# Performance work log

Measured on AMD Instinct MI355X. Metric: run time of the kernel, lower is better.

Reference implementation:

```python
import jax, jax.numpy as jnp
import numpy as np

KS = 3          # deform kernel size
N = KS * KS     # 9 sampling taps per pixel
PAD = 1         # zero padding applied before sampling (nn.ZeroPad2d)
BN_EPS = 1e-5


def conv2d(x, w, b=None, stride=1, padding=0):
    out = jax.lax.conv_general_dilated(
        x, w, (stride, stride), [(padding, padding)] * 2,
        dimension_numbers=('NCHW', 'OIHW', 'NCHW'))
    if b is not None:
        out = out + b[None, :, None, None]
    return out


def setup_inputs() -> dict:
    key = jax.random.key(0)
    ks = jax.random.split(key, 6)
    inC, outC = 128, 256
    B, H, W = 8, 64, 64

    def kaiming(k, shape):
        fan_in = shape[1] * shape[2] * shape[3]
        return jax.random.normal(k, shape, jnp.float32) / np.float32(np.sqrt(fan_in))

    return {
        'x': jax.random.normal(ks[0], (B, inC, H, W), jnp.float32),
        'w_offset': kaiming(ks[1], (2 * N, inC, 3, 3)) * 0.1,  # small offsets, realistic
        'b_offset': jnp.zeros((2 * N,), jnp.float32),
        'w_mask': kaiming(ks[2], (N, inC, 3, 3)),
        'b_mask': jnp.zeros((N,), jnp.float32),
        'w_conv': kaiming(ks[3], (outC, inC, KS, KS)),
        'bn_gamma': jnp.ones((outC,), jnp.float32),
        'bn_beta': jnp.zeros((outC,), jnp.float32),
        'bn_mean': jax.random.normal(ks[4], (outC,), jnp.float32) * 0.1,
        'bn_var': jnp.ones((outC,), jnp.float32) + jax.random.uniform(ks[5], (outC,), jnp.float32) * 0.1,
    }


def deform_conv(x, w_offset, b_offset, w_mask, b_mask, w_conv):
    B, C, H, W = x.shape
    dt = x.dtype

    offset = conv2d(x, w_offset, b_offset, 1, 1)               # (B, 2N, H, W)
    m = jax.nn.sigmoid(conv2d(x, w_mask, b_mask, 1, 1))        # (B, N, H, W)

    # kernel grid offsets p_n (first N channels = rows, last N = cols)
    rng = jnp.arange(-(KS - 1) // 2, (KS - 1) // 2 + 1, dtype=dt)
    pnx, pny = jnp.meshgrid(rng, rng, indexing='ij')
    p_n = jnp.concatenate([pnx.reshape(-1), pny.reshape(-1)])[None, :, None, None]

    # base positions p_0 (torch impl starts at 1, sampling on padded input)
    p0x = jnp.broadcast_to(jnp.arange(1, H + 1, dtype=dt)[:, None], (H, W))
    p0y = jnp.broadcast_to(jnp.arange(1, W + 1, dtype=dt)[None, :], (H, W))
    p_0 = jnp.concatenate([jnp.tile(p0x[None], (N, 1, 1)),
                           jnp.tile(p0y[None], (N, 1, 1))])[None]  # (1, 2N, H, W)

    p = (offset + p_n + p_0).transpose(0, 2, 3, 1)             # (B, H, W, 2N)

    xp = jnp.pad(x, ((0, 0), (0, 0), (PAD, PAD), (PAD, PAD)))
    Hp, Wp = H + 2 * PAD, W + 2 * PAD

    px, py = p[..., :N], p[..., N:]
    fx, fy = jnp.floor(px), jnp.floor(py)
    q_lt_x = jnp.clip(fx, 0, Hp - 1)
    q_lt_y = jnp.clip(fy, 0, Wp - 1)
    q_rb_x = jnp.clip(fx + 1, 0, Hp - 1)
    q_rb_y = jnp.clip(fy + 1, 0, Wp - 1)
    px = jnp.clip(px, 0, Hp - 1)
    py = jnp.clip(py, 0, Wp - 1)

    # bilinear weights (faithful to the reference torch formulas)
    g_lt = (1 + (q_lt_x - px)) * (1 + (q_lt_y - py))
    g_rb = (1 - (q_rb_x - px)) * (1 - (q_rb_y - py))
    g_lb = (1 + (q_lt_x - px)) * (1 - (q_rb_y - py))
    g_rt = (1 - (q_rb_x - px)) * (1 + (q_lt_y - py))

    xp_flat = xp.reshape(B, C, Hp * Wp)

    def gather(qx, qy):
        idx = (qx.astype(jnp.int32) * Wp + qy.astype(jnp.int32)).reshape(B, 1, -1)
        out = jnp.take_along_axis(xp_flat,
                                  jnp.broadcast_to(idx, (B, C, idx.shape[-1])), axis=2)
        return out.reshape(B, C, H, W, N)

    x_off = (g_lt[:, None] * gather(q_lt_x, q_lt_y)
             + g_rb[:, None] * gather(q_rb_x, q_rb_y)
             + g_lb[:, None] * gather(q_lt_x, q_rb_y)
             + g_rt[:, None] * gather(q_rb_x, q_lt_y))       # (B, C, H, W, N)

    x_off = x_off * m.transpose(0, 2, 3, 1)[:, None]          # modulation

    # (B,C,H,W,ks,ks) -> (B,C,H*ks,W*ks)  (equivalent to _reshape_x_offset)
    x_off = x_off.reshape(B, C, H, W, KS, KS).transpose(0, 1, 2, 4, 3, 5)
    x_off = x_off.reshape(B, C, H * KS, W * KS)

    return conv2d(x_off, w_conv, None, KS, 0)                 # (B, outC, H, W)


def reference(x, w_offset, b_offset, w_mask, b_mask, w_conv,
              bn_gamma, bn_beta, bn_mean, bn_var):
    y = deform_conv(x, w_offset, b_offset, w_mask, b_mask, w_conv)
    inv = jax.lax.rsqrt(bn_var + BN_EPS)
    scale = (bn_gamma * inv)[None, :, None, None]
    shift = (bn_beta - bn_mean * bn_gamma * inv)[None, :, None, None]
    return jax.nn.relu(y * scale + shift)
```

## Files before the change

### kernel.cpp

```cpp
#include <hip/hip_runtime.h>
#include <math.h>

#define BB 8
#define CC 128
#define HH 64
#define WW 64
#define NPTS 9
#define OUTC 256
#define HW (HH*WW)
#define KTOT (CC*NPTS)
#define BK 288
#define AP 290
#define WROWS 6

typedef __attribute__((ext_vector_type(8))) short bf16x8;
typedef __attribute__((ext_vector_type(4))) float f32x4;

__device__ unsigned short g_wT[OUTC * KTOT];
__device__ unsigned short g_woT[32 * KTOT];

__device__ __forceinline__ unsigned short f2bf(float f) {
    unsigned int u = __builtin_bit_cast(unsigned int, f);
    unsigned int r = (u + 0x7FFFu + ((u >> 16) & 1u)) >> 16;
    return (unsigned short)r;
}

__device__ __forceinline__ unsigned cvtpk(float lo, float hi) {
    unsigned r;
    asm("v_cvt_pk_bf16_f32 %0, %1, %2" : "=v"(r) : "v"(lo), "v"(hi));
    return r;
}
__device__ __forceinline__ float bflo(unsigned w) { return __builtin_bit_cast(float, w << 16); }
__device__ __forceinline__ float bfhi(unsigned w) { return __builtin_bit_cast(float, w & 0xFFFF0000u); }

__device__ __forceinline__ int orig_k(int k) {
    int cb = k / BK, r = k % BK;
    int pair = r / 18, r2 = r % 18;
    int n = r2 >> 1, half = r2 & 1;
    return (cb * 32 + pair * 2 + half) * NPTS + n;
}

__global__ __launch_bounds__(256) void prep_kernel(
    const float* __restrict__ wo, const float* __restrict__ wm,
    const float* __restrict__ wc)
{
    int idx = blockIdx.x * 256 + threadIdx.x;
    const int T1 = 32 * KTOT;
    if (idx < T1) {
        int nn = idx / KTOT, k = idx - nn * KTOT;
        int ok = orig_k(k);
        float v = (nn < 18) ? wo[nn * KTOT + ok]
                            : (nn < 27 ? wm[(nn - 18) * KTOT + ok] : 0.f);
        g_woT[idx] = f2bf(v);
    } else if (idx < T1 + OUTC * KTOT) {
        int j = idx - T1;
        int oc = j / KTOT, k = j - oc * KTOT;
        g_wT[j] = f2bf(wc[oc * KTOT + orig_k(k)]);
    }
}

struct PF { uint2 w[WROWS]; };

__device__ __forceinline__ void issue(PF& pf, const float* __restrict__ xb,
                                      int h, int cb, int tid) {
    if (cb < 0 || cb > 3) return;
    int q = tid >> 6, col = tid & 63;
    const float* base = xb + (size_t)(cb * 32 + 4 * q) * HW + col;
    #pragma unroll
    for (int r = 0; r < WROWS; ++r) {
        int gr = h - 2 + r;
        bool v = (gr >= 0) & (gr < HH);
        float a0 = v ? base[0 * HW + gr * WW] : 0.f;
        float a1 = v ? base[1 * HW + gr * WW] : 0.f;
        float a2 = v ? base[2 * HW + gr * WW] : 0.f;
        float a3 = v ? base[3 * HW + gr * WW] : 0.f;
        pf.w[r].x = cvtpk(a0, a1);
        pf.w[r].y = cvtpk(a2, a3);
    }
}

__device__ __forceinline__ void commit(uint2* win, const PF& pf, int tid) {
    uint2* wp = win + (tid >> 6) * 384 + (tid & 63);
    #pragma unroll
    for (int r = 0; r < WROWS; ++r) wp[r * 64] = pf.w[r];
}

__global__ __launch_bounds__(512) __attribute__((amdgpu_waves_per_eu(4, 4)))
void fused_kernel(
    const float* __restrict__ x,
    const float* __restrict__ b_offset, const float* __restrict__ b_mask,
    const float* __restrict__ bn_gamma, const float* __restrict__ bn_beta,
    const float* __restrict__ bn_mean,  const float* __restrict__ bn_var,
    float* __restrict__ out)
{
    __shared__ unsigned short Atile[64][AP];
    __shared__ uint2 win[8 * 384];
    __shared__ float4 gtab[NPTS][64];
    __shared__ uint2  otab[NPTS][64];
    float* ovf = (float*)&Atile[0][0];

    int bid = blockIdx.x;
    int blk = (bid & 7) * 64 + (bid >> 3);
    int b = blk >> 6, h = blk & 63;
    int tid  = threadIdx.x;
    int lane = tid & 63;
    int wv   = __builtin_amdgcn_readfirstlane(tid >> 6);
    int l15  = lane & 15;
    int kg   = lane >> 4;
    int spix = lane;

    const float* xb = x + (size_t)b * CC * HW;
    unsigned* AtU = (unsigned*)&Atile[0][0];

    int mi_a = wv & 3, nf_a = wv >> 2;
    f32x4 s1acc = {0.f, 0.f, 0.f, 0.f};

    PF pf; issue(pf, xb, h, 0, tid);
    for (int cb = 0; cb < 4; ++cb) {
        commit(win, pf, tid);
        {
            const uint2* base = win + wv * 384;
            #pragma unroll
            for (int tap = 0; tap < 9; ++tap) {
                int ky = tap / 3, kx = tap % 3;
                int col  = spix + kx - 1;
                int colc = min(max(col, 0), WW - 1);
                uint2 v = base[(ky + 1) * 64 + colc];
                bool cv = (col >= 0) & (col < WW);
                AtU[spix * 145 + (2 * wv) * 9 + tap]     = cv ? v.x : 0u;
                AtU[spix * 145 + (2 * wv + 1) * 9 + tap] = cv ? v.y : 0u;
            }
        }
        issue(pf, xb, h, (cb < 3) ? cb + 1 : 2, tid);
        __syncthreads();
        __builtin_amdgcn_s_setprio(1);
        for (int q = 0; q < 9; ++q) {
            int koff = q * 32 + kg * 8;
            bf16x8 af = *(const bf16x8*)&Atile[mi_a * 16 + l15][koff];
            int nn = nf_a * 16 + l15;
            bf16x8 bfr = *(const bf16x8*)&g_woT[nn * KTOT + cb * BK + koff];
            s1acc = __builtin_amdgcn_mfma_f32_16x16x32_bf16(af, bfr, s1acc, 0, 0, 0);
        }
        __builtin_amdgcn_s_setprio(0);
        __syncthreads();
    }

    #pragma unroll
    for (int j = 0; j < 4; ++j) {
        float val = s1acc[j];
        int nn   = nf_a * 16 + l15;
        int pixl = mi_a * 16 + kg * 4 + j;
        if (nn < 9) {
            ovf[nn * 64 + pixl] = val + b_offset[nn] + (float)(nn / 3 - 1) + (float)(h + 1);
        } else if (nn < 18) {
            int n = nn - 9;
            ovf[576 + n * 64 + pixl] = val + b_offset[nn] + (float)(n % 3 - 1) + (float)(pixl + 1);
        } else if (nn < 27) {
            int n = nn - 18;
            float sg = val + b_mask[n];
            ovf[1152 + n * 64 + pixl] = 1.f / (1.f + expf(-sg));
        }
    }
    __syncthreads();

    for (int n = wv; n < NPTS; n += 8) {
        int t = lane;
        float px = ovf[n * 64 + t];
        float py = ovf[576 + n * 64 + t];
        float m  = ovf[1152 + n * 64 + t];
        float fx = floorf(px), fy = floorf(py);
        float qltx = fminf(fmaxf(fx,       0.f), 65.f);
        float qlty = fminf(fmaxf(fy,       0.f), 65.f);
        float qrbx = fminf(fmaxf(fx + 1.f, 0.f), 65.f);
        float qrby = fminf(fmaxf(fy + 1.f, 0.f), 65.f);
        float pxc  = fminf(fmaxf(px, 0.f), 65.f);
        float pyc  = fminf(fmaxf(py, 0.f), 65.f);
        float glt = (1.f + (qltx - pxc)) * (1.f + (qlty - pyc)) * m;
        float grb = (1.f - (qrbx - pxc)) * (1.f - (qrby - pyc)) * m;
        float glb = (1.f + (qltx - pxc)) * (1.f - (qrby - pyc)) * m;
        float grt = (1.f - (qrbx - pxc)) * (1.f + (qlty - pyc)) * m;
        int i0 = (int)qltx - 1, j0 = (int)qlty - 1;
        int i1 = (int)qrbx - 1, j1 = (int)qrby - 1;
        bool v00 = (i0 >= 0) & (i0 < HH) & (j0 >= 0) & (j0 < WW);
        bool v11 = (i1 >= 0) & (i1 < HH) & (j1 >= 0) & (j1 < WW);
        bool v01 = (i0 >= 0) & (i0 < HH) & (j1 >= 0) & (j1 < WW);
        bool v10 = (i1 >= 0) & (i1 < HH) & (j0 >= 0) & (j0 < WW);
        float4 g;
        g.x = v00 ? glt : 0.f;
        g.y = v11 ? grb : 0.f;
        g.z = v01 ? glb : 0.f;
        g.w = v10 ? grt : 0.f;
        gtab[n][t] = g;
        bool okr0 = ((i0 >= h - 2) & (i0 <= h + 3)) | !(v00 | v01);
        bool okr1 = ((i1 >= h - 2) & (i1 <= h + 3)) | !(v11 | v10);
        bool ok = okr0 & okr1;
        int r0w = min(max(i0 - (h - 2), 0), WROWS - 1);
        int r1w = min(max(i1 - (h - 2), 0), WROWS - 1);
        int r0g = min(max(i0, 0), HH - 1);
        int r1g = min(max(i1, 0), HH - 1);
        int j0c = min(max(j0, 0), WW - 1);
        int j1c = min(max(j1, 0), WW - 1);
        int o  = ok ? (r0w * WW + j0c) : (r0g * WW + j0c);
        int dr = ok ? (r1w - r0w) : (r1g - r0g);
        int dj = j1c - j0c;
        unsigned o00 = (unsigned)o;
        unsigned o11 = (unsigned)(o + dr * WW + dj);
        unsigned o01 = (unsigned)(o + dj);
        unsigned o10 = (unsigned)(o + dr * WW);
        uint2 ot;
        ot.x = (o00 | (ok ? 0u : 0x8000u)) | (o11 << 16);
        ot.y = o01 | (o10 << 16);
        otab[n][t] = ot;
    }
    __syncthreads();

    f32x4 acc[4][2];
    #pragma unroll
    for (int mi = 0; mi < 4; ++mi)
        #pragma unroll
        for (int ni = 0; ni < 2; ++ni)
            acc[mi][ni] = (f32x4){0.f, 0.f, 0.f, 0.f};

    int oc0 = wv * 32;

    for (int j = 0; j < 4; ++j) {
        int cb = 3 - j;
        if (j > 0) {
            commit(win, pf, tid);
            issue(pf, xb, h, cb - 1, tid);
        }
        {
            const uint2* baseq = win + wv * 384;
            const float* xg = xb + (size_t)(cb * 32 + 4 * wv) * HW;
            #pragma unroll
            for (int n = 0; n < NPTS; ++n) {
                float4 g  = gtab[n][spix];
                uint2  ot = otab[n][spix];
                int o00 = ot.x & 0x7FFF;
                int o11 = ot.x >> 16;
                int o01 = ot.y & 0xFFFF;
                int o10 = ot.y >> 16;
                float v0, v1, v2, v3;
                if (!(ot.x & 0x8000u)) {
                    uint2 c00 = baseq[o00];
                    uint2 c11 = baseq[o11];
                    uint2 c01 = baseq[o01];
                    uint2 c10 = baseq[o10];
                    v0 =       g.x * bflo(c00.x);
                    v0 = fmaf(g.y, bflo(c11.x), v0);
                    v0 = fmaf(g.z, bflo(c01.x), v0);
                    v0 = fmaf(g.w, bflo(c10.x), v0);
                    v1 =       g.x * bfhi(c00.x);
                    v1 = fmaf(g.y, bfhi(c11.x), v1);
                    v1 = fmaf(g.z, bfhi(c01.x), v1);
                    v1 = fmaf(g.w, bfhi(c10.x), v1);
                    v2 =       g.x * bflo(c00.y);
                    v2 = fmaf(g.y, bflo(c11.y), v2);
                    v2 = fmaf(g.z, bflo(c01.y), v2);
                    v2 = fmaf(g.w, bflo(c10.y), v2);
                    v3 =       g.x * bfhi(c00.y);
                    v3 = fmaf(g.y, bfhi(c11.y), v3);
                    v3 = fmaf(g.z, bfhi(c01.y), v3);
                    v3 = fmaf(g.w, bfhi(c10.y), v3);
                } else {
                    const float* x0 = xg;
                    const float* x1 = xg + HW;
                    const float* x2 = xg + 2 * HW;
                    const float* x3 = xg + 3 * HW;
                    v0 = g.x*x0[o00]; v0 = fmaf(g.y, x0[o11], v0); v0 = fmaf(g.z, x0[o01], v0); v0 = fmaf(g.w, x0[o10], v0);
                    v1 = g.x*x1[o00]; v1 = fmaf(g.y, x1[o11], v1); v1 = fmaf(g.z, x1[o01], v1); v1 = fmaf(g.w, x1[o10], v1);
                    v2 = g.x*x2[o00]; v2 = fmaf(g.y, x2[o11], v2); v2 = fmaf(g.z, x2[o01], v2); v2 = fmaf(g.w, x2[o10], v2);
                    v3 = g.x*x3[o00]; v3 = fmaf(g.y, x3[o11], v3); v3 = fmaf(g.z, x3[o01], v3); v3 = fmaf(g.w, x3[o10], v3);
                }
                AtU[spix * 145 + (2 * wv) * 9 + n]     = cvtpk(v0, v1);
                AtU[spix * 145 + (2 * wv + 1) * 9 + n] = cvtpk(v2, v3);
            }
        }
        __syncthreads();
        __builtin_amdgcn_s_setprio(1);
        for (int q = 0; q < 9; ++q) {
            int koff = q * 32 + kg * 8;
            bf16x8 af[4];
            #pragma unroll
            for (int mi = 0; mi < 4; ++mi)
                af[mi] = *(const bf16x8*)&Atile[mi * 16 + l15][koff];
            #pragma unroll
            for (int ni = 0; ni < 2; ++ni) {
                int oc = oc0 + ni * 16 + l15;
                bf16x8 bfr = *(const bf16x8*)&g_wT[oc * KTOT + cb * BK + koff];
                #pragma unroll
                for (int mi = 0; mi < 4; ++mi)
                    acc[mi][ni] = __builtin_amdgcn_mfma_f32_16x16x32_bf16(af[mi], bfr, acc[mi][ni], 0, 0, 0);
            }
        }
        __builtin_amdgcn_s_setprio(0);
        __syncthreads();
    }

    #pragma unroll
    for (int ni = 0; ni < 2; ++ni) {
        int oc = oc0 + ni * 16 + l15;
        float inv   = 1.f / sqrtf(bn_var[oc] + 1e-5f);
        float scale = bn_gamma[oc] * inv;
        float shift = bn_beta[oc] - bn_mean[oc] * scale;
        float* op = out + ((size_t)b * OUTC + oc) * HW + h * WW + kg * 4;
        #pragma unroll
        for (int mi = 0; mi < 4; ++mi) {
            f32x4 o4;
            #pragma unroll
            for (int j = 0; j < 4; ++j) {
                float v = fmaf(acc[mi][ni][j], scale, shift);
                o4[j] = v > 0.f ? v : 0.f;
            }
            *(f32x4*)(op + mi * 16) = o4;
        }
    }
}

extern "C" void kernel_launch(void* const* d_in, const int* in_sizes, int n_in,
                              void* d_out, int out_size, void* d_ws, size_t ws_size,
                              hipStream_t stream) {
    (void)in_sizes; (void)n_in; (void)out_size; (void)d_ws; (void)ws_size;
    const float* x        = (const float*)d_in[0];
    const float* w_offset = (const float*)d_in[1];
    const float* b_offset = (const float*)d_in[2];
    const float* w_mask   = (const float*)d_in[3];
    const float* b_mask   = (const float*)d_in[4];
    const float* w_conv   = (const float*)d_in[5];
    const float* bn_gamma = (const float*)d_in[6];
    const float* bn_beta  = (const float*)d_in[7];
    const float* bn_mean  = (const float*)d_in[8];
    const float* bn_var   = (const float*)d_in[9];
    float* out = (float*)d_out;

    int prep_elems = 32 * KTOT + OUTC * KTOT;
    prep_kernel<<<(prep_elems + 255) / 256, 256, 0, stream>>>(w_offset, w_mask, w_conv);
    fused_kernel<<<BB * HH, 512, 0, stream>>>(x, b_offset, b_mask,
                                              bn_gamma, bn_beta, bn_mean, bn_var, out);
}
```

Before: 81.29 us.

## Split each output row across two blocks of 32 pixels for more parallelism

Each block now handles half of an output row (32 pixels) instead of the full 64, doubling the grid to 1024 blocks. Each wave now builds two channels for 32 pixels instead of four channels for 64 pixels, and only four waves run the offset/mask MFMA stage. Shared memory per block shrinks, and the waves-per-EU hint is relaxed to allow more occupancy. The cost is that the input window load and the weight B-fragment reads are duplicated across the two halves, and each wave now does half as many MFMAs per B-fragment load.

```diff
diff --git a/kernel.cpp b/kernel.cpp
--- a/kernel.cpp
+++ b/kernel.cpp
@@ -85,7 +85,7 @@
     for (int r = 0; r < WROWS; ++r) wp[r * 64] = pf.w[r];
 }
 
-__global__ __launch_bounds__(512) __attribute__((amdgpu_waves_per_eu(4, 4)))
+__global__ __launch_bounds__(512) __attribute__((amdgpu_waves_per_eu(4, 8)))
 void fused_kernel(
     const float* __restrict__ x,
     const float* __restrict__ b_offset, const float* __restrict__ b_mask,
@@ -93,130 +93,139 @@
     const float* __restrict__ bn_mean,  const float* __restrict__ bn_var,
     float* __restrict__ out)
 {
-    __shared__ unsigned short Atile[64][AP];
+    __shared__ unsigned short Atile[32][AP];
     __shared__ uint2 win[8 * 384];
-    __shared__ float4 gtab[NPTS][64];
-    __shared__ uint2  otab[NPTS][64];
+    __shared__ float4 gtab[NPTS][32];
+    __shared__ uint2  otab[NPTS][32];
     float* ovf = (float*)&Atile[0][0];
 
     int bid = blockIdx.x;
-    int blk = (bid & 7) * 64 + (bid >> 3);
-    int b = blk >> 6, h = blk & 63;
+    int b = bid & 7;
+    int rr = bid >> 3;
+    int h = rr >> 1, half = rr & 1;
     int tid  = threadIdx.x;
     int lane = tid & 63;
     int wv   = __builtin_amdgcn_readfirstlane(tid >> 6);
     int l15  = lane & 15;
     int kg   = lane >> 4;
-    int spix = lane;
+    int p    = lane & 31;
+    int ps   = lane >> 5;
+    int pairIdx = wv * 2 + ps;
 
     const float* xb = x + (size_t)b * CC * HW;
     unsigned* AtU = (unsigned*)&Atile[0][0];
-
-    int mi_a = wv & 3, nf_a = wv >> 2;
+    const unsigned* wu = (const unsigned*)(win + wv * 384);
+
+    int mi_a = wv & 1, nf_a = (wv >> 1) & 1;
     f32x4 s1acc = {0.f, 0.f, 0.f, 0.f};
 
     PF pf; issue(pf, xb, h, 0, tid);
     for (int cb = 0; cb < 4; ++cb) {
         commit(win, pf, tid);
         {
-            const uint2* base = win + wv * 384;
             #pragma unroll
             for (int tap = 0; tap < 9; ++tap) {
                 int ky = tap / 3, kx = tap % 3;
-                int col  = spix + kx - 1;
-                int colc = min(max(col, 0), WW - 1);
-                uint2 v = base[(ky + 1) * 64 + colc];
-                bool cv = (col >= 0) & (col < WW);
-                AtU[spix * 145 + (2 * wv) * 9 + tap]     = cv ? v.x : 0u;
-                AtU[spix * 145 + (2 * wv + 1) * 9 + tap] = cv ? v.y : 0u;
+                int gcol = half * 32 + p + kx - 1;
+                int colc = min(max(gcol, 0), WW - 1);
+                unsigned w = wu[((ky + 1) * 64 + colc) * 2 + ps];
+                w = (gcol >= 0 && gcol < WW) ? w : 0u;
+                AtU[p * 145 + pairIdx * 9 + tap] = w;
             }
         }
         issue(pf, xb, h, (cb < 3) ? cb + 1 : 2, tid);
         __syncthreads();
         __builtin_amdgcn_s_setprio(1);
-        for (int q = 0; q < 9; ++q) {
-            int koff = q * 32 + kg * 8;
-            bf16x8 af = *(const bf16x8*)&Atile[mi_a * 16 + l15][koff];
-            int nn = nf_a * 16 + l15;
-            bf16x8 bfr = *(const bf16x8*)&g_woT[nn * KTOT + cb * BK + koff];
-            s1acc = __builtin_amdgcn_mfma_f32_16x16x32_bf16(af, bfr, s1acc, 0, 0, 0);
+        if (wv < 4) {
+            for (int q = 0; q < 9; ++q) {
+                int koff = q * 32 + kg * 8;
+                bf16x8 af = *(const bf16x8*)&Atile[mi_a * 16 + l15][koff];
+                int nn = nf_a * 16 + l15;
+                bf16x8 bfr = *(const bf16x8*)&g_woT[nn * KTOT + cb * BK + koff];
+                s1acc = __builtin_amdgcn_mfma_f32_16x16x32_bf16(af, bfr, s1acc, 0, 0, 0);
+            }
         }
         __builtin_amdgcn_s_setprio(0);
         __syncthreads();
     }
 
+    if (wv < 4) {
+        #pragma unroll
+        for (int j = 0; j < 4; ++j) {
+            float val = s1acc[j];
+            int nn   = nf_a * 16 + l15;
+            int pixl = mi_a * 16 + kg * 4 + j;
+            if (nn < 9) {
+                ovf[nn * 32 + pixl] = val + b_offset[nn] + (float)(nn / 3 - 1) + (float)(h + 1);
+            } else if (nn < 18) {
+                int n = nn - 9;
+                ovf[288 + n * 32 + pixl] = val + b_offset[nn] + (float)(n % 3 - 1)
+                                         + (float)(half * 32 + pixl + 1);
+            } else if (nn < 27) {
+                int n = nn - 18;
+                float sg = val + b_mask[n];
+                ovf[576 + n * 32 + pixl] = 1.f / (1.f + expf(-sg));
+            }
+        }
+    }
+    __syncthreads();
+
+    for (int n = wv; n < NPTS; n += 8) {
+        if (lane < 32) {
+            int t = lane;
+            float px = ovf[n * 32 + t];
+            float py = ovf[288 + n * 32 + t];
+            float m  = ovf[576 + n * 32 + t];
+            float fx = floorf(px), fy = floorf(py);
+            float qltx = fminf(fmaxf(fx,       0.f), 65.f);
+            float qlty = fminf(fmaxf(fy,       0.f), 65.f);
+            float qrbx = fminf(fmaxf(fx + 1.f, 0.f), 65.f);
+            float qrby = fminf(fmaxf(fy + 1.f, 0.f), 65.f);
+            float pxc  = fminf(fmaxf(px, 0.f), 65.f);
+            float pyc  = fminf(fmaxf(py, 0.f), 65.f);
+            float glt = (1.f + (qltx - pxc)) * (1.f + (qlty - pyc)) * m;
+            float grb = (1.f - (qrbx - pxc)) * (1.f - (qrby - pyc)) * m;
+            float glb = (1.f + (qltx - pxc)) * (1.f - (qrby - pyc)) * m;
+            float grt = (1.f - (qrbx - pxc)) * (1.f + (qlty - pyc)) * m;
+            int i0 = (int)qltx - 1, j0 = (int)qlty - 1;
+            int i1 = (int)qrbx - 1, j1 = (int)qrby - 1;
+            bool v00 = (i0 >= 0) & (i0 < HH) & (j0 >= 0) & (j0 < WW);
+            bool v11 = (i1 >= 0) & (i1 < HH) & (j1 >= 0) & (j1 < WW);
+            bool v01 = (i0 >= 0) & (i0 < HH) & (j1 >= 0) & (j1 < WW);
+            bool v10 = (i1 >= 0) & (i1 < HH) & (j0 >= 0) & (j0 < WW);
+            float4 g;
+            g.x = v00 ? glt : 0.f;
+            g.y = v11 ? grb : 0.f;
+            g.z = v01 ? glb : 0.f;
+            g.w = v10 ? grt : 0.f;
+            gtab[n][t] = g;
+            bool okr0 = ((i0 >= h - 2) & (i0 <= h + 3)) | !(v00 | v01);
+            bool okr1 = ((i1 >= h - 2) & (i1 <= h + 3)) | !(v11 | v10);
+            bool ok = okr0 & okr1;
+            int r0w = min(max(i0 - (h - 2), 0), WROWS - 1);
+            int r1w = min(max(i1 - (h - 2), 0), WROWS - 1);
+            int r0g = min(max(i0, 0), HH - 1);
+            int r1g = min(max(i1, 0), HH - 1);
+            int j0c = min(max(j0, 0), WW - 1);
+            int j1c = min(max(j1, 0), WW - 1);
+            int o  = ok ? (r0w * WW + j0c) : (r0g * WW + j0c);
+            int dr = ok ? (r1w - r0w) : (r1g - r0g);
+            int dj = j1c - j0c;
+            unsigned o00 = (unsigned)o;
+            unsigned o11 = (unsigned)(o + dr * WW + dj);
+            unsigned o01 = (unsigned)(o + dj);
+            unsigned o10 = (unsigned)(o + dr * WW);
+            uint2 ot;
+            ot.x = (o00 | (ok ? 0u : 0x8000u)) | (o11 << 16);
+            ot.y = o01 | (o10 << 16);
+            otab[n][t] = ot;
+        }
+    }
+    __syncthreads();
+
+    f32x4 acc[2][2];
     #pragma unroll
-    for (int j = 0; j < 4; ++j) {
-        float val = s1acc[j];
-        int nn   = nf_a * 16 + l15;
-        int pixl = mi_a * 16 + kg * 4 + j;
-        if (nn < 9) {
-            ovf[nn * 64 + pixl] = val + b_offset[nn] + (float)(nn / 3 - 1) + (float)(h + 1);
-        } else if (nn < 18) {
-            int n = nn - 9;
-            ovf[576 + n * 64 + pixl] = val + b_offset[nn] + (float)(n % 3 - 1) + (float)(pixl + 1);
-        } else if (nn < 27) {
-            int n = nn - 18;
-            float sg = val + b_mask[n];
-            ovf[1152 + n * 64 + pixl] = 1.f / (1.f + expf(-sg));
-        }
-    }
-    __syncthreads();
-
-    for (int n = wv; n < NPTS; n += 8) {
-        int t = lane;
-        float px = ovf[n * 64 + t];
-        float py = ovf[576 + n * 64 + t];
-        float m  = ovf[1152 + n * 64 + t];
-        float fx = floorf(px), fy = floorf(py);
-        float qltx = fminf(fmaxf(fx,       0.f), 65.f);
-        float qlty = fminf(fmaxf(fy,       0.f), 65.f);
-        float qrbx = fminf(fmaxf(fx + 1.f, 0.f), 65.f);
-        float qrby = fminf(fmaxf(fy + 1.f, 0.f), 65.f);
-        float pxc  = fminf(fmaxf(px, 0.f), 65.f);
-        float pyc  = fminf(fmaxf(py, 0.f), 65.f);
-        float glt = (1.f + (qltx - pxc)) * (1.f + (qlty - pyc)) * m;
-        float grb = (1.f - (qrbx - pxc)) * (1.f - (qrby - pyc)) * m;
-        float glb = (1.f + (qltx - pxc)) * (1.f - (qrby - pyc)) * m;
-        float grt = (1.f - (qrbx - pxc)) * (1.f + (qlty - pyc)) * m;
-        int i0 = (int)qltx - 1, j0 = (int)qlty - 1;
-        int i1 = (int)qrbx - 1, j1 = (int)qrby - 1;
-        bool v00 = (i0 >= 0) & (i0 < HH) & (j0 >= 0) & (j0 < WW);
-        bool v11 = (i1 >= 0) & (i1 < HH) & (j1 >= 0) & (j1 < WW);
-        bool v01 = (i0 >= 0) & (i0 < HH) & (j1 >= 0) & (j1 < WW);
-        bool v10 = (i1 >= 0) & (i1 < HH) & (j0 >= 0) & (j0 < WW);
-        float4 g;
-        g.x = v00 ? glt : 0.f;
-        g.y = v11 ? grb : 0.f;
-        g.z = v01 ? glb : 0.f;
-        g.w = v10 ? grt : 0.f;
-        gtab[n][t] = g;
-        bool okr0 = ((i0 >= h - 2) & (i0 <= h + 3)) | !(v00 | v01);
-        bool okr1 = ((i1 >= h - 2) & (i1 <= h + 3)) | !(v11 | v10);
-        bool ok = okr0 & okr1;
-        int r0w = min(max(i0 - (h - 2), 0), WROWS - 1);
-        int r1w = min(max(i1 - (h - 2), 0), WROWS - 1);
-        int r0g = min(max(i0, 0), HH - 1);
-        int r1g = min(max(i1, 0), HH - 1);
-        int j0c = min(max(j0, 0), WW - 1);
-        int j1c = min(max(j1, 0), WW - 1);
-        int o  = ok ? (r0w * WW + j0c) : (r0g * WW + j0c);
-        int dr = ok ? (r1w - r0w) : (r1g - r0g);
-        int dj = j1c - j0c;
-        unsigned o00 = (unsigned)o;
-        unsigned o11 = (unsigned)(o + dr * WW + dj);
-        unsigned o01 = (unsigned)(o + dj);
-        unsigned o10 = (unsigned)(o + dr * WW);
-        uint2 ot;
-        ot.x = (o00 | (ok ? 0u : 0x8000u)) | (o11 << 16);
-        ot.y = o01 | (o10 << 16);
-        otab[n][t] = ot;
-    }
-    __syncthreads();
-
-    f32x4 acc[4][2];
-    #pragma unroll
-    for (int mi = 0; mi < 4; ++mi)
+    for (int mi = 0; mi < 2; ++mi)
         #pragma unroll
         for (int ni = 0; ni < 2; ++ni)
             acc[mi][ni] = (f32x4){0.f, 0.f, 0.f, 0.f};
@@ -230,66 +239,57 @@
             issue(pf, xb, h, cb - 1, tid);
         }
         {
-            const uint2* baseq = win + wv * 384;
-            const float* xg = xb + (size_t)(cb * 32 + 4 * wv) * HW;
+            const float* xgA = xb + (size_t)(cb * 32 + pairIdx * 2) * HW;
+            const float* xgB = xgA + HW;
             #pragma unroll
             for (int n = 0; n < NPTS; ++n) {
-                float4 g  = gtab[n][spix];
-                uint2  ot = otab[n][spix];
+                float4 g  = gtab[n][p];
+                uint2  ot = otab[n][p];
                 int o00 = ot.x & 0x7FFF;
                 int o11 = ot.x >> 16;
                 int o01 = ot.y & 0xFFFF;
                 int o10 = ot.y >> 16;
-                float v0, v1, v2, v3;
+                float v0, v1;
                 if (!(ot.x & 0x8000u)) {
-                    uint2 c00 = baseq[o00];
-                    uint2 c11 = baseq[o11];
-                    uint2 c01 = baseq[o01];
-                    uint2 c10 = baseq[o10];
-                    v0 =       g.x * bflo(c00.x);
-                    v0 = fmaf(g.y, bflo(c11.x), v0);
-                    v0 = fmaf(g.z, bflo(c01.x), v0);
-                    v0 = fmaf(g.w, bflo(c10.x), v0);
-                    v1 =       g.x * bfhi(c00.x);
-                    v1 = fmaf(g.y, bfhi(c11.x), v1);
-                    v1 = fmaf(g.z, bfhi(c01.x), v1);
-                    v1 = fmaf(g.w, bfhi(c10.x), v1);
-                    v2 =       g.x * bflo(c00.y);
-                    v2 = fmaf(g.y, bflo(c11.y), v2);
-                    v2 = fmaf(g.z, bflo(c01.y), v2);
-                    v2 = fmaf(g.w, bflo(c10.y), v2);
-                    v3 =       g.x * bfhi(c00.y);
-                    v3 = fmaf(g.y, bfhi(c11.y), v3);
-                    v3 = fmaf(g.z, bfhi(c01.y), v3);
-                    v3 = fmaf(g.w, bfhi(c10.y), v3);
+                    unsigned w00 = wu[o00 * 2 + ps];
+                    unsigned w11 = wu[o11 * 2 + ps];
+                    unsigned w01 = wu[o01 * 2 + ps];
+                    unsigned w10 = wu[o10 * 2 + ps];
+                    v0 =       g.x * bflo(w00);
+                    v0 = fmaf(g.y, bflo(w11), v0);
+                    v0 = fmaf(g.z, bflo(w01), v0);
+                    v0 = fmaf(g.w, bflo(w10), v0);
+                    v1 =       g.x * bfhi(w00);
+                    v1 = fmaf(g.y, bfhi(w11), v1);
+                    v1 = fmaf(g.z, bfhi(w01), v1);
+                    v1 = fmaf(g.w, bfhi(w10), v1);
                 } else {
-                    const float* x0 = xg;
-                    const float* x1 = xg + HW;
-                    const float* x2 = xg + 2 * HW;
-                    const float* x3 = xg + 3 * HW;
-                    v0 = g.x*x0[o00]; v0 = fmaf(g.y, x0[o11], v0); v0 = fmaf(g.z, x0[o01], v0); v0 = fmaf(g.w, x0[o10], v0);
-                    v1 = g.x*x1[o00]; v1 = fmaf(g.y, x1[o11], v1); v1 = fmaf(g.z, x1[o01], v1); v1 = fmaf(g.w, x1[o10], v1);
-                    v2 = g.x*x2[o00]; v2 = fmaf(g.y, x2[o11], v2); v2 = fmaf(g.z, x2[o01], v2); v2 = fmaf(g.w, x2[o10], v2);
-                    v3 = g.x*x3[o00]; v3 = fmaf(g.y, x3[o11], v3); v3 = fmaf(g.z, x3[o01], v3); v3 = fmaf(g.w, x3[o10], v3);
+                    v0 =       g.x * xgA[o00];
+                    v0 = fmaf(g.y, xgA[o11], v0);
+                    v0 = fmaf(g.z, xgA[o01], v0);
+                    v0 = fmaf(g.w, xgA[o10], v0);
+                    v1 =       g.x * xgB[o00];
+                    v1 = fmaf(g.y, xgB[o11], v1);
+                    v1 = fmaf(g.z, xgB[o01], v1);
+                    v1 = fmaf(g.w, xgB[o10], v1);
                 }
-                AtU[spix * 145 + (2 * wv) * 9 + n]     = cvtpk(v0, v1);
-                AtU[spix * 145 + (2 * wv + 1) * 9 + n] = cvtpk(v2, v3);
+                AtU[p * 145 + pairIdx * 9 + n] = cvtpk(v0, v1);
             }
         }
         __syncthreads();
         __builtin_amdgcn_s_setprio(1);
         for (int q = 0; q < 9; ++q) {
             int koff = q * 32 + kg * 8;
-            bf16x8 af[4];
-            #pragma unroll
-            for (int mi = 0; mi < 4; ++mi)
+            bf16x8 af[2];
+            #pragma unroll
+            for (int mi = 0; mi < 2; ++mi)
                 af[mi] = *(const bf16x8*)&Atile[mi * 16 + l15][koff];
             #pragma unroll
             for (int ni = 0; ni < 2; ++ni) {
                 int oc = oc0 + ni * 16 + l15;
                 bf16x8 bfr = *(const bf16x8*)&g_wT[oc * KTOT + cb * BK + koff];
                 #pragma unroll
-                for (int mi = 0; mi < 4; ++mi)
+                for (int mi = 0; mi < 2; ++mi)
                     acc[mi][ni] = __builtin_amdgcn_mfma_f32_16x16x32_bf16(af[mi], bfr, acc[mi][ni], 0, 0, 0);
             }
         }
@@ -303,14 +303,14 @@
         float inv   = 1.f / sqrtf(bn_var[oc] + 1e-5f);
         float scale = bn_gamma[oc] * inv;
         float shift = bn_beta[oc] - bn_mean[oc] * scale;
-        float* op = out + ((size_t)b * OUTC + oc) * HW + h * WW + kg * 4;
+        float* op = out + ((size_t)b * OUTC + oc) * HW + h * WW + half * 32 + kg * 4;
         #pragma unroll
-        for (int mi = 0; mi < 4; ++mi) {
+        for (int mi = 0; mi < 2; ++mi) {
             f32x4 o4;
             #pragma unroll
-            for (int j = 0; j < 4; ++j) {
-                float v = fmaf(acc[mi][ni][j], scale, shift);
-                o4[j] = v > 0.f ? v : 0.f;
+            for (int jj = 0; jj < 4; ++jj) {
+                float v = fmaf(acc[mi][ni][jj], scale, shift);
+                o4[jj] = v > 0.f ? v : 0.f;
             }
             *(f32x4*)(op + mi * 16) = o4;
         }
@@ -335,6 +335,6 @@
 
     int prep_elems = 32 * KTOT + OUTC * KTOT;
     prep_kernel<<<(prep_elems + 255) / 256, 256, 0, stream>>>(w_offset, w_mask, w_conv);
-    fused_kernel<<<BB * HH, 512, 0, stream>>>(x, b_offset, b_mask,
-                                              bn_gamma, bn_beta, bn_mean, bn_var, out);
-}
+    fused_kernel<<<BB * HH * 2, 512, 0, stream>>>(x, b_offset, b_mask,
+                                                  bn_gamma, bn_beta, bn_mean, bn_var, out);
+}
```

Measured after the change: 133.3 us. 1.64x slower.
